# Optimization experiments

Hardware: AMD Instinct MI355X
Metric: run time of the kernel (lower is better)

Reference implementation:

```python
import jax, jax.numpy as jnp
import numpy as np

N, L, H, DH = 4, 1024, 16, 64
D = H * DH  # 1024
DFF = 4 * D
NEG_INF = jnp.float32(-1e30)  # used via actual -inf per torch masked_fill


def layer_norm(x, g, b, eps=1e-5):
    mu = jnp.mean(x, axis=-1, keepdims=True)
    var = jnp.mean(jnp.square(x - mu), axis=-1, keepdims=True)
    return (x - mu) * jax.lax.rsqrt(var + eps) * g + b


def mha(q_in, k_in, Wq, Wk, Wv, mask, padding_mask):
    # q_in: (N,Lq,D), k_in: (N,Lk,D); Linear weights (D,D), out = x @ W.T
    n, Lq, _ = q_in.shape
    Lk = k_in.shape[1]
    q = jnp.einsum('nld,od->nlo', q_in, Wq).reshape(n, Lq, H, DH)
    k = jnp.einsum('nld,od->nlo', k_in, Wk).reshape(n, Lk, H, DH)
    v = jnp.einsum('nld,od->nlo', k_in, Wv).reshape(n, Lk, H, DH)
    # per-sample scaling = sqrt(#non-padded keys)
    scaling = jnp.sqrt(jnp.sum(~padding_mask, axis=-1).astype(q.dtype))  # (N,)
    score = jnp.einsum('nqhd,nkhd->nhqk', q, k) / scaling[:, None, None, None]
    if mask is not None:
        score = jnp.where(mask[None, None, :, :], -jnp.inf, score)
    score = jnp.where(padding_mask[:, None, None, :], -jnp.inf, score)
    p = jax.nn.softmax(score, axis=-1)
    out = jnp.einsum('nhqk,nkhd->nqhd', p, v).reshape(n, Lq, D)
    return out


def setup_inputs() -> dict:
    key = jax.random.key(0)
    ks = jax.random.split(key, 16)
    s = 0.02
    inp = {
        'encoded': jax.random.normal(ks[0], (N, L, D), jnp.float32),
        'Y': jax.random.normal(ks[1], (N, L, D), jnp.float32),
        # causal mask: True above diagonal -> attention set to -inf
        'mask': ~jnp.tril(jnp.ones((L, L), dtype=bool)),
        # suffix padding with varied per-sample lengths (all >= 1)
        'padding_mask': jnp.arange(L)[None, :] >= jnp.array([L, 3 * L // 4, L // 2, 7 * L // 8])[:, None],
        # masked self-attention projections
        'Wq1': jax.random.normal(ks[2], (D, D), jnp.float32) * s,
        'Wk1': jax.random.normal(ks[3], (D, D), jnp.float32) * s,
        'Wv1': jax.random.normal(ks[4], (D, D), jnp.float32) * s,
        'g1': jnp.ones((D,), jnp.float32), 'b1': jnp.zeros((D,), jnp.float32),
        # cross-attention projections
        'Wq2': jax.random.normal(ks[5], (D, D), jnp.float32) * s,
        'Wk2': jax.random.normal(ks[6], (D, D), jnp.float32) * s,
        'Wv2': jax.random.normal(ks[7], (D, D), jnp.float32) * s,
        'g2': jnp.ones((D,), jnp.float32), 'b2': jnp.zeros((D,), jnp.float32),
        # FFN
        'We': jax.random.normal(ks[8], (DFF, D), jnp.float32) * s,
        'be': jnp.zeros((DFF,), jnp.float32),
        'Wc': jax.random.normal(ks[9], (D, DFF), jnp.float32) * s,
        'bc': jnp.zeros((D,), jnp.float32),
        'g3': jnp.ones((D,), jnp.float32), 'b3': jnp.zeros((D,), jnp.float32),
    }
    return inp


def reference(encoded, Y, mask, padding_mask,
              Wq1, Wk1, Wv1, g1, b1,
              Wq2, Wk2, Wv2, g2, b2,
              We, be, Wc, bc, g3, b3):
    # masked self-attention + residual + LN (dropout=0 -> identity)
    res = Y
    a = mha(Y, Y, Wq1, Wk1, Wv1, mask, padding_mask)
    Y = layer_norm(a + res, g1, b1)
    # cross-attention (no causal mask) + residual + LN
    res = Y
    a = mha(Y, encoded, Wq2, Wk2, Wv2, None, padding_mask)
    Y = layer_norm(a + res, g2, b2)
    # FFN + residual + LN
    res = Y
    h = jax.nn.relu(jnp.einsum('nld,fd->nlf', Y, We) + be)
    h = jnp.einsum('nlf,df->nld', h, Wc) + bc
    Y = layer_norm(h + res, g3, b3)
    return Y
```

## Files before the change

### kernel.cpp

```cpp
#include <hip/hip_runtime.h>
#include <stdint.h>

#define NB 4
#define LS 1024
#define HH 16
#define DHD 64
#define DM 1024
#define DF 4096
#define QKS 2048

typedef unsigned short u16;
typedef __attribute__((ext_vector_type(4))) float f32x4;
typedef __attribute__((ext_vector_type(8))) __bf16 bf16x8;
typedef __attribute__((ext_vector_type(8))) unsigned short u16x8;

__device__ __forceinline__ u16 f2bf(float f) {
  union { float f; uint32_t u; } v; v.f = f;
  uint32_t u = v.u;
  return (u16)((u + 0x7fffu + ((u >> 16) & 1u)) >> 16);
}

__device__ __forceinline__ bf16x8 ldb8(const u16* p) {
  u16x8 r = *(const u16x8*)p;
  return __builtin_bit_cast(bf16x8, r);
}

__device__ __forceinline__ void gload_lds16(const u16* g, u16* l) {
  __builtin_amdgcn_global_load_lds((const __attribute__((address_space(1))) void*)g,
                                   (__attribute__((address_space(3))) void*)l,
                                   16, 0, 0);
}

#define WAITV8() asm volatile("s_waitcnt vmcnt(8)" ::: "memory")
#define WAITV0() asm volatile("s_waitcnt vmcnt(0)" ::: "memory")
#define WAITLGKM() asm volatile("s_waitcnt lgkmcnt(0)" ::: "memory")
#define PHASE_BARRIER()                        \
  do {                                         \
    WAITLGKM();                                \
    __builtin_amdgcn_sched_barrier(0);         \
    __builtin_amdgcn_s_barrier();              \
    __builtin_amdgcn_sched_barrier(0);         \
  } while (0)

__global__ void prep_kernel(const uint32_t* __restrict__ pm, int* lens, float* iscl) {
  __shared__ int flagByte;
  __shared__ int red[256];
  const int tid = threadIdx.x, n = blockIdx.x;
  if (tid == 0) flagByte = 0;
  __syncthreads();
  int f = 0;
  for (int w = tid; w < (NB * LS) / 4; w += 256) {
    uint32_t u = pm[w];
    if (u != 0u && u != 1u && u != 0x3f800000u) f = 1;
  }
  if (f) atomicOr(&flagByte, 1);
  __syncthreads();
  int c = 0;
  if (flagByte) {
    const uint8_t* pb = (const uint8_t*)pm;
    for (int l = tid; l < LS; l += 256) c += (pb[n * LS + l] == 0) ? 1 : 0;
  } else {
    for (int l = tid; l < LS; l += 256) c += (pm[n * LS + l] == 0) ? 1 : 0;
  }
  red[tid] = c;
  __syncthreads();
  for (int s = 128; s > 0; s >>= 1) {
    if (tid < s) red[tid] += red[tid + s];
    __syncthreads();
  }
  if (tid == 0) { lens[n] = red[0]; iscl[n] = 1.0f / sqrtf((float)red[0]); }
}

__global__ void cvt_all(const float* s0, u16* d0, const float* s1, u16* d1,
                        const float* s2, u16* d2, const float* s3, u16* d3,
                        const float* s4, u16* d4, const float* s5, u16* d5,
                        const float* s6, u16* d6, const float* s7, u16* d7,
                        const float* s8, u16* d8, const float* s9, u16* d9) {
  const int total = 5767168;
  int i = blockIdx.x * 256 + threadIdx.x;
  for (; i < total; i += gridDim.x * 256) {
    const float* s; u16* d; int j;
    if (i < 1048576)      { s = s0; d = d0; j = i; }
    else if (i < 2097152) { s = s1; d = d1; j = i - 1048576; }
    else if (i < 2359296) { s = s2; d = d2; j = i - 2097152; }
    else if (i < 2621440) { s = s3; d = d3; j = i - 2359296; }
    else if (i < 2883584) { s = s4; d = d4; j = i - 2621440; }
    else if (i < 3145728) { s = s5; d = d5; j = i - 2883584; }
    else if (i < 3407872) { s = s6; d = d6; j = i - 3145728; }
    else if (i < 3670016) { s = s7; d = d7; j = i - 3407872; }
    else if (i < 4718592) { s = s8; d = d8; j = i - 3670016; }
    else                  { s = s9; d = d9; j = i - 4718592; }
    float4 fv = ((const float4*)s)[j];
    ushort4 o;
    o.x = f2bf(fv.x); o.y = f2bf(fv.y); o.z = f2bf(fv.z); o.w = f2bf(fv.w);
    ((ushort4*)d)[j] = o;
  }
}

template <int MODE>
__global__ __launch_bounds__(512, 2) void gemm8(
    const u16* __restrict__ P0, const u16* __restrict__ P1,
    const u16* __restrict__ PW, const float* __restrict__ bias,
    void* __restrict__ O0, void* __restrict__ O1,
    void* __restrict__ O2, void* __restrict__ O3) {
  extern __shared__ u16 lds[];
  constexpr int NT = 16;
  const int bm = blockIdx.x;
  const int tid = threadIdx.x;
  const int wid = tid >> 6, lane = tid & 63;
  const int lrow = lane & 15, lgrp = lane >> 4;
  const int wm = wid >> 2, wn = wid & 3;

  const u16* Asrc; const u16* Bsrc; int lda, ldb;
  if constexpr (MODE == 0) {
    Asrc = P0 + (size_t)bm * 256 * DM; lda = DM;
    Bsrc = PW + (size_t)blockIdx.y * 256 * DM; ldb = DM;
  } else if constexpr (MODE == 1) {
    const int z = blockIdx.z;
    Asrc = P0 + (size_t)bm * 256 * DF + z * 1024; lda = DF;
    Bsrc = PW + (size_t)blockIdx.y * 256 * DF + z * 1024; ldb = DF;
  } else {
    const int bnt = blockIdx.y;
    Asrc = (bnt < 12 ? P0 : P1) + (size_t)bm * 256 * DM; lda = DM;
    const int wrow = (bnt < 12) ? bnt * 256 : 4096 + (bnt - 12) * 256;
    Bsrc = PW + (size_t)wrow * DM; ldb = DM;
  }

  int srow[2], skk[2];
#pragma unroll
  for (int i = 0; i < 2; i++) {
    const int c = (i * 8 + wid) * 64 + lane;
    const int pair = c >> 3;
    const int ue = ((c & 7) * 8) ^ ((pair & 7) << 3);
    srow[i] = pair * 2 + (ue >> 5);
    skk[i] = ue & 31;
  }
  const int dslot0 = wid * 512;
  const int dslot1 = (8 + wid) * 512;

  f32x4 acc[2][4][4] = {};

  auto STAGE_A = [&](int kt, int buf, int kh) {
    const int ks = kt < NT ? kt : NT - 1;
    gload_lds16(Asrc + (size_t)srow[0] * lda + ks * 64 + kh * 32 + skk[0],
                lds + buf * 16384 + kh * 8192 + dslot0);
    gload_lds16(Asrc + (size_t)srow[1] * lda + ks * 64 + kh * 32 + skk[1],
                lds + buf * 16384 + kh * 8192 + dslot1);
  };
  auto STAGE_B = [&](int kt, int buf, int kh) {
    const int ks = kt < NT ? kt : NT - 1;
    gload_lds16(Bsrc + (size_t)srow[0] * ldb + ks * 64 + kh * 32 + skk[0],
                lds + 32768 + buf * 16384 + kh * 8192 + dslot0);
    gload_lds16(Bsrc + (size_t)srow[1] * ldb + ks * 64 + kh * 32 + skk[1],
                lds + 32768 + buf * 16384 + kh * 8192 + dslot1);
  };
  auto LDA = [&](int buf, int kh, int mh, bf16x8* a) {
#pragma unroll
    for (int m = 0; m < 4; m++) {
      const int row = wm * 128 + mh * 64 + m * 16 + lrow;
      const int idx = buf * 16384 + kh * 8192 + (row >> 1) * 64 +
                      ((((row & 1) << 5) + (lgrp << 3)) ^ (((row >> 1) & 7) << 3));
      a[m] = ldb8(lds + idx);
    }
  };
  auto LDB = [&](int buf, int kh, bf16x8* b) {
#pragma unroll
    for (int nn = 0; nn < 4; nn++) {
      const int row = wn * 64 + nn * 16 + lrow;
      const int idx = 32768 + buf * 16384 + kh * 8192 + (row >> 1) * 64 +
                      ((((row & 1) << 5) + (lgrp << 3)) ^ (((row >> 1) & 7) << 3));
      b[nn] = ldb8(lds + idx);
    }
  };
  auto MFMA16 = [&](f32x4 (&a4)[4][4], bf16x8* af, bf16x8* bk) {
    __builtin_amdgcn_s_setprio(1);
#pragma unroll
    for (int m = 0; m < 4; m++)
#pragma unroll
      for (int nn = 0; nn < 4; nn++)
        a4[m][nn] = __builtin_amdgcn_mfma_f32_16x16x32_bf16(af[m], bk[nn], a4[m][nn], 0, 0, 0);
    __builtin_amdgcn_s_setprio(0);
  };

  STAGE_A(0, 0, 0); STAGE_B(0, 0, 0);
  STAGE_A(0, 0, 1); STAGE_B(0, 0, 1);
  STAGE_A(1, 1, 0); STAGE_B(1, 1, 0);
  WAITV8();
  __builtin_amdgcn_s_barrier();
  __builtin_amdgcn_sched_barrier(0);

  for (int t = 0; t < NT; t++) {
    const int b = t & 1;
    bf16x8 af[4], bk[4];
    LDA(b, 0, 0, af); LDB(b, 0, bk);
    STAGE_A(t + 1, b ^ 1, 1);
    PHASE_BARRIER();
    MFMA16(acc[0], af, bk);
    LDA(b, 0, 1, af);
    STAGE_B(t + 1, b ^ 1, 1);
    WAITV8();
    PHASE_BARRIER();
    MFMA16(acc[1], af, bk);
    LDA(b, 1, 0, af); LDB(b, 1, bk);
    STAGE_A(t + 2, b, 0);
    PHASE_BARRIER();
    MFMA16(acc[0], af, bk);
    LDA(b, 1, 1, af);
    STAGE_B(t + 2, b, 0);
    WAITV8();
    PHASE_BARRIER();
    MFMA16(acc[1], af, bk);
  }
  WAITV0();

#pragma unroll
  for (int mh = 0; mh < 2; mh++)
#pragma unroll
    for (int m = 0; m < 4; m++) {
      const int grow0 = bm * 256 + wm * 128 + mh * 64 + m * 16 + lgrp * 4;
#pragma unroll
      for (int nn = 0; nn < 4; nn++) {
        const int col_l = wn * 64 + nn * 16 + lrow;
        f32x4 v = acc[mh][m][nn];
        if constexpr (MODE == 0) {
          const int col = blockIdx.y * 256 + col_l;
          const float bv = bias[col];
#pragma unroll
          for (int r = 0; r < 4; r++) {
            float x = v[r] + bv;
            x = x > 0.0f ? x : 0.0f;
            ((u16*)O0)[(size_t)(grow0 + r) * DF + col] = f2bf(x);
          }
        } else if constexpr (MODE == 1) {
          float* C = (float*)O0 + (size_t)blockIdx.z * ((size_t)NB * LS * DM);
          const int col = blockIdx.y * 256 + col_l;
#pragma unroll
          for (int r = 0; r < 4; r++) C[(size_t)(grow0 + r) * DM + col] = v[r];
        } else {
          const int bnt = blockIdx.y;
          const int nidx = grow0 >> 10, l0 = grow0 & 1023;
          if (bnt < 8) {
            const int col = bnt * 256 + col_l;
#pragma unroll
            for (int r = 0; r < 4; r++)
              ((u16*)O0)[(size_t)(grow0 + r) * QKS + col] = f2bf(v[r]);
          } else if (bnt < 12) {
            const int vc = (bnt - 8) * 256 + col_l;
            ushort4 o;
            o.x = f2bf(v[0]); o.y = f2bf(v[1]); o.z = f2bf(v[2]); o.w = f2bf(v[3]);
            *(ushort4*)((u16*)O1 + (((size_t)(nidx * HH + (vc >> 6)) * DHD + (vc & 63)) << 10) + l0) = o;
          } else {
            const int col = 1024 + (bnt - 12) * 256 + col_l;
#pragma unroll
            for (int r = 0; r < 4; r++)
              ((u16*)O2)[(size_t)(grow0 + r) * QKS + col] = f2bf(v[r]);
          }
        }
      }
    }
}

__global__ __launch_bounds__(256) void gemm_qv(const u16* __restrict__ Ya,
                                               const u16* __restrict__ Ea,
                                               const u16* __restrict__ Wq,
                                               const u16* __restrict__ Wv,
                                               u16* __restrict__ QKb,
                                               u16* __restrict__ VtB) {
  __shared__ u16 Al[128 * 32];
  __shared__ u16 Bl[128 * 32];
  const int tid = threadIdx.x;
  const int bm = blockIdx.x, bnr = blockIdx.y;
  const bool isV = bnr >= 8;
  const int bn = isV ? bnr - 8 : bnr;
  const int wave = tid >> 6, lane = tid & 63;
  const int lrow = lane & 15, lgrp = lane >> 4;
  const int wr = (wave >> 1) * 64, wc = (wave & 1) * 64;
  f32x4 acc[4][4] = {};
  const u16* Ab = (isV ? Ea : Ya) + (size_t)bm * 128 * DM;
  const u16* Bb = (isV ? Wv : Wq) + (size_t)bn * 128 * DM;
  {
    const int c0 = wave, c1 = wave + 4;
    const int r0 = c0 * 16 + (lane >> 2), r1 = c1 * 16 + (lane >> 2);
    const int scc = (lane & 3) * 8;
    const u16* Ag0 = Ab + (size_t)r0 * DM + scc;
    const u16* Ag1 = Ab + (size_t)r1 * DM + scc;
    const u16* Bg0 = Bb + (size_t)r0 * DM + scc;
    const u16* Bg1 = Bb + (size_t)r1 * DM + scc;
    u16* Ad0 = Al + c0 * 512;
    u16* Ad1 = Al + c1 * 512;
    u16* Bd0 = Bl + c0 * 512;
    u16* Bd1 = Bl + c1 * 512;
    for (int kb = 0; kb < DM; kb += 32) {
      gload_lds16(Ag0, Ad0);
      gload_lds16(Ag1, Ad1);
      gload_lds16(Bg0, Bd0);
      gload_lds16(Bg1, Bd1);
      Ag0 += 32; Ag1 += 32; Bg0 += 32; Bg1 += 32;
      __syncthreads();
      bf16x8 af[4], bfr[4];
#pragma unroll
      for (int m = 0; m < 4; m++) af[m] = ldb8(Al + (wr + m * 16 + lrow) * 32 + lgrp * 8);
#pragma unroll
      for (int nn = 0; nn < 4; nn++) bfr[nn] = ldb8(Bl + (wc + nn * 16 + lrow) * 32 + lgrp * 8);
#pragma unroll
      for (int m = 0; m < 4; m++)
#pragma unroll
        for (int nn = 0; nn < 4; nn++)
          acc[m][nn] = __builtin_amdgcn_mfma_f32_16x16x32_bf16(af[m], bfr[nn], acc[m][nn], 0, 0, 0);
      __syncthreads();
    }
  }
#pragma unroll
  for (int m = 0; m < 4; m++) {
    const int row0 = bm * 128 + wr + m * 16 + lgrp * 4;
    const int nidx = row0 >> 10, l0 = row0 & (LS - 1);
#pragma unroll
    for (int nn = 0; nn < 4; nn++) {
      const int col = bn * 128 + wc + nn * 16 + lrow;
      if (!isV) {
#pragma unroll
        for (int r = 0; r < 4; r++)
          QKb[(size_t)(row0 + r) * QKS + col] = f2bf(acc[m][nn][r]);
      } else {
        const int hh = col >> 6, dd = col & 63;
        ushort4 o;
        o.x = f2bf(acc[m][nn][0]); o.y = f2bf(acc[m][nn][1]);
        o.z = f2bf(acc[m][nn][2]); o.w = f2bf(acc[m][nn][3]);
        *(ushort4*)(VtB + (((size_t)(nidx * HH + hh) * DHD + dd) << 10) + l0) = o;
      }
    }
  }
}

template <bool CAUSAL>
__global__ __launch_bounds__(256) void attn_kernel(const u16* __restrict__ QK,
                                                   const u16* __restrict__ Vt,
                                                   float* __restrict__ Out,
                                                   const int* __restrict__ lens,
                                                   const float* __restrict__ iscl) {
  __shared__ u16 Kl[64 * 72];
  __shared__ u16 Vl[64 * 72];
  __shared__ u16 Pl[4][16 * 72];
  const int n = blockIdx.z, h = blockIdx.y, qb = blockIdx.x * 64;
  const int tid = threadIdx.x, wave = tid >> 6, lane = tid & 63;
  const int lrow = lane & 15, lgrp = lane >> 4;
  const int len = lens[n];
  const float isc = iscl[n];
  const int qrow = qb + wave * 16 + lrow;
  const u16* qptr = QK + ((size_t)(n * LS + qrow)) * QKS + h * DHD + lgrp * 8;
  bf16x8 qf0 = ldb8(qptr);
  bf16x8 qf1 = ldb8(qptr + 32);
  f32x4 oacc[4] = {};
  float m_run[4], l_run[4];
#pragma unroll
  for (int r = 0; r < 4; r++) { m_run[r] = -1e30f; l_run[r] = 0.0f; }
  const int kend = CAUSAL ? (len < qb + 64 ? len : qb + 64) : len;
  const int srow = tid >> 3, sc = (tid & 7) * 8;
  const u16* kg_base = QK + 1024 + ((size_t)(n * LS)) * QKS + h * DHD + sc;
  const u16* vg_base = Vt + ((size_t)((n * HH + h) * DHD) + srow) * LS + sc;
  u16* pw = Pl[wave];
  for (int kb = 0; kb < kend; kb += 64) {
    __syncthreads();
#pragma unroll
    for (int i = 0; i < 2; i++) {
      const int row = srow + i * 32;
      u16x8 kv = *(const u16x8*)(kg_base + (size_t)(kb + row) * QKS);
      *(u16x8*)(Kl + row * 72 + sc) = kv;
      u16x8 vv = *(const u16x8*)(vg_base + (size_t)(i * 32) * LS + kb);
      *(u16x8*)(Vl + row * 72 + sc) = vv;
    }
    __syncthreads();
    f32x4 s[4];
#pragma unroll
    for (int st = 0; st < 4; st++) {
      const u16* kr = Kl + (st * 16 + lrow) * 72 + lgrp * 8;
      bf16x8 kf0 = ldb8(kr);
      bf16x8 kf1 = ldb8(kr + 32);
      f32x4 z = {};
      z = __builtin_amdgcn_mfma_f32_16x16x32_bf16(qf0, kf0, z, 0, 0, 0);
      s[st] = __builtin_amdgcn_mfma_f32_16x16x32_bf16(qf1, kf1, z, 0, 0, 0);
    }
    const int q_r = qb + wave * 16 + lgrp * 4;
#pragma unroll
    for (int st = 0; st < 4; st++) {
      const int k = kb + st * 16 + lrow;
#pragma unroll
      for (int r = 0; r < 4; r++) {
        float v = s[st][r] * isc;
        bool ok = (k < len) && (!CAUSAL || k <= q_r + r);
        s[st][r] = ok ? v : -1e30f;
      }
    }
#pragma unroll
    for (int r = 0; r < 4; r++) {
      float mx = fmaxf(fmaxf(s[0][r], s[1][r]), fmaxf(s[2][r], s[3][r]));
      mx = fmaxf(mx, __shfl_xor(mx, 1));
      mx = fmaxf(mx, __shfl_xor(mx, 2));
      mx = fmaxf(mx, __shfl_xor(mx, 4));
      mx = fmaxf(mx, __shfl_xor(mx, 8));
      float mn = fmaxf(m_run[r], mx);
      float fac = __expf(m_run[r] - mn);
      m_run[r] = mn;
      float sm = 0.0f;
#pragma unroll
      for (int st = 0; st < 4; st++) {
        float p = __expf(s[st][r] - mn);
        s[st][r] = p;
        sm += p;
      }
      sm += __shfl_xor(sm, 1);
      sm += __shfl_xor(sm, 2);
      sm += __shfl_xor(sm, 4);
      sm += __shfl_xor(sm, 8);
      l_run[r] = l_run[r] * fac + sm;
#pragma unroll
      for (int dt = 0; dt < 4; dt++) oacc[dt][r] *= fac;
    }
#pragma unroll
    for (int st = 0; st < 4; st++)
#pragma unroll
      for (int r = 0; r < 4; r++)
        pw[(lgrp * 4 + r) * 72 + st * 16 + lrow] = f2bf(s[st][r]);
#pragma unroll
    for (int ks = 0; ks < 2; ks++) {
      bf16x8 pf = ldb8(pw + lrow * 72 + ks * 32 + lgrp * 8);
#pragma unroll
      for (int dt = 0; dt < 4; dt++) {
        bf16x8 vf = ldb8(Vl + (dt * 16 + lrow) * 72 + ks * 32 + lgrp * 8);
        oacc[dt] = __builtin_amdgcn_mfma_f32_16x16x32_bf16(pf, vf, oacc[dt], 0, 0, 0);
      }
    }
  }
#pragma unroll
  for (int r = 0; r < 4; r++) {
    float inv = 1.0f / l_run[r];
    const int row = qb + wave * 16 + lgrp * 4 + r;
    float* op = Out + ((size_t)(n * LS + row)) * DM + h * DHD;
#pragma unroll
    for (int dt = 0; dt < 4; dt++) op[dt * 16 + lrow] = oacc[dt][r] * inv;
  }
}

__global__ __launch_bounds__(256) void ln_kernel(const float* __restrict__ a,
                                                 const float* __restrict__ res,
                                                 const float* __restrict__ g,
                                                 const float* __restrict__ bta,
                                                 float* __restrict__ outf,
                                                 u16* __restrict__ outb) {
  const int row = blockIdx.x, tid = threadIdx.x;
  float4 x = ((const float4*)(a + (size_t)row * DM))[tid];
  float4 rr = ((const float4*)(res + (size_t)row * DM))[tid];
  x.x += rr.x; x.y += rr.y; x.z += rr.z; x.w += rr.w;
  float s = x.x + x.y + x.z + x.w;
  float s2 = x.x * x.x + x.y * x.y + x.z * x.z + x.w * x.w;
#pragma unroll
  for (int m = 1; m < 64; m <<= 1) { s += __shfl_xor(s, m); s2 += __shfl_xor(s2, m); }
  __shared__ float sm[8];
  const int wv = tid >> 6;
  if ((tid & 63) == 0) { sm[wv] = s; sm[4 + wv] = s2; }
  __syncthreads();
  s = sm[0] + sm[1] + sm[2] + sm[3];
  s2 = sm[4] + sm[5] + sm[6] + sm[7];
  const float mean = s * (1.0f / (float)DM);
  const float var = s2 * (1.0f / (float)DM) - mean * mean;
  const float inv = rsqrtf(var + 1e-5f);
  float4 gg = ((const float4*)g)[tid];
  float4 bb = ((const float4*)bta)[tid];
  float4 y;
  y.x = (x.x - mean) * inv * gg.x + bb.x;
  y.y = (x.y - mean) * inv * gg.y + bb.y;
  y.z = (x.z - mean) * inv * gg.z + bb.z;
  y.w = (x.w - mean) * inv * gg.w + bb.w;
  ((float4*)(outf + (size_t)row * DM))[tid] = y;
  if (outb) {
    ushort4 o;
    o.x = f2bf(y.x); o.y = f2bf(y.y); o.z = f2bf(y.z); o.w = f2bf(y.w);
    ((ushort4*)(outb + (size_t)row * DM))[tid] = o;
  }
}

__global__ __launch_bounds__(256) void ln_final(const float* __restrict__ part,
                                                const float* __restrict__ bias,
                                                const float* __restrict__ res,
                                                const float* __restrict__ g,
                                                const float* __restrict__ bta,
                                                float* __restrict__ outf) {
  const int row = blockIdx.x, tid = threadIdx.x;
  const size_t PS = (size_t)NB * LS * DM;
  float4 x = ((const float4*)(part + (size_t)row * DM))[tid];
  float4 p1 = ((const float4*)(part + PS + (size_t)row * DM))[tid];
  float4 p2 = ((const float4*)(part + 2 * PS + (size_t)row * DM))[tid];
  float4 p3 = ((const float4*)(part + 3 * PS + (size_t)row * DM))[tid];
  float4 bb4 = ((const float4*)bias)[tid];
  float4 rr = ((const float4*)(res + (size_t)row * DM))[tid];
  x.x += p1.x + p2.x + p3.x + bb4.x + rr.x;
  x.y += p1.y + p2.y + p3.y + bb4.y + rr.y;
  x.z += p1.z + p2.z + p3.z + bb4.z + rr.z;
  x.w += p1.w + p2.w + p3.w + bb4.w + rr.w;
  float s = x.x + x.y + x.z + x.w;
  float s2 = x.x * x.x + x.y * x.y + x.z * x.z + x.w * x.w;
#pragma unroll
  for (int m = 1; m < 64; m <<= 1) { s += __shfl_xor(s, m); s2 += __shfl_xor(s2, m); }
  __shared__ float sm[8];
  const int wv = tid >> 6;
  if ((tid & 63) == 0) { sm[wv] = s; sm[4 + wv] = s2; }
  __syncthreads();
  s = sm[0] + sm[1] + sm[2] + sm[3];
  s2 = sm[4] + sm[5] + sm[6] + sm[7];
  const float mean = s * (1.0f / (float)DM);
  const float var = s2 * (1.0f / (float)DM) - mean * mean;
  const float inv = rsqrtf(var + 1e-5f);
  float4 gg = ((const float4*)g)[tid];
  float4 bb = ((const float4*)bta)[tid];
  float4 y;
  y.x = (x.x - mean) * inv * gg.x + bb.x;
  y.y = (x.y - mean) * inv * gg.y + bb.y;
  y.z = (x.z - mean) * inv * gg.z + bb.z;
  y.w = (x.w - mean) * inv * gg.w + bb.w;
  ((float4*)(outf + (size_t)row * DM))[tid] = y;
}

extern "C" void kernel_launch(void* const* d_in, const int* in_sizes, int n_in,
                              void* d_out, int out_size, void* d_ws, size_t ws_size,
                              hipStream_t stream) {
  const float* enc = (const float*)d_in[0];
  const float* Yin = (const float*)d_in[1];
  const uint32_t* pmask = (const uint32_t*)d_in[3];
  const float* Wq1 = (const float*)d_in[4];
  const float* Wk1 = (const float*)d_in[5];
  const float* Wv1 = (const float*)d_in[6];
  const float* g1 = (const float*)d_in[7];
  const float* b1 = (const float*)d_in[8];
  const float* Wq2 = (const float*)d_in[9];
  const float* Wk2 = (const float*)d_in[10];
  const float* Wv2 = (const float*)d_in[11];
  const float* g2 = (const float*)d_in[12];
  const float* b2 = (const float*)d_in[13];
  const float* We = (const float*)d_in[14];
  const float* be = (const float*)d_in[15];
  const float* Wc = (const float*)d_in[16];
  const float* bc = (const float*)d_in[17];
  const float* g3 = (const float*)d_in[18];
  const float* b3 = (const float*)d_in[19];

  const size_t ACT = (size_t)NB * LS * DM;
  const size_t WSZ = (size_t)DM * DM;
  const size_t WFF = (size_t)DF * DM;
  const size_t HID = (size_t)NB * LS * DF;

  char* ws = (char*)d_ws;
  size_t off = 0;
  auto alloc = [&](size_t bytes) -> void* {
    void* p = ws + off;
    off += (bytes + 255) & ~(size_t)255;
    return p;
  };
  int* lens = (int*)alloc(64);
  float* iscl = (float*)alloc(64);
  u16* Ybf = (u16*)alloc(ACT * 2);
  u16* Ebf = (u16*)alloc(ACT * 2);
  u16* W6 = (u16*)alloc(WSZ * 6 * 2);
  u16* Web = (u16*)alloc(WFF * 2);
  u16* Wcb = (u16*)alloc(WFF * 2);
  size_t region0 = off;
  u16* QKa = (u16*)alloc((size_t)NB * LS * QKS * 2);
  u16* VtA = (u16*)alloc(ACT * 2);
  u16* QKb = (u16*)alloc((size_t)NB * LS * QKS * 2);
  u16* VtB = (u16*)alloc(ACT * 2);
  float* aout = (float*)alloc(ACT * 4);
  float* y2 = (float*)alloc(ACT * 4);
  float* part = (float*)(ws + region0);
  float* y3 = (float*)alloc(ACT * 4);
  u16* Hb = (u16*)alloc(HID * 2);

  prep_kernel<<<NB, 256, 0, stream>>>(pmask, lens, iscl);
  cvt_all<<<2048, 256, 0, stream>>>(Yin, Ybf, enc, Ebf,
                                    Wq1, W6 + 0 * WSZ, Wk1, W6 + 1 * WSZ,
                                    Wv1, W6 + 2 * WSZ, Wq2, W6 + 3 * WSZ,
                                    Wk2, W6 + 4 * WSZ, Wv2, W6 + 5 * WSZ,
                                    We, Web, Wc, Wcb);

  dim3 blk(256);
  gemm8<2><<<dim3(16, 16), 512, 131072, stream>>>(Ybf, Ebf, W6, nullptr,
                                                  QKa, VtA, QKb, VtB);
  attn_kernel<true><<<dim3(16, 16, 4), blk, 0, stream>>>(QKa, VtA, aout, lens, iscl);
  ln_kernel<<<NB * LS, 256, 0, stream>>>(aout, Yin, g1, b1, y2, Ybf);
  gemm_qv<<<dim3(32, 16), blk, 0, stream>>>(Ybf, Ebf, W6 + 3 * WSZ, W6 + 5 * WSZ,
                                            QKb, VtB);
  attn_kernel<false><<<dim3(16, 16, 4), blk, 0, stream>>>(QKb, VtB, aout, lens, iscl);
  ln_kernel<<<NB * LS, 256, 0, stream>>>(aout, y2, g2, b2, y3, Ebf);
  gemm8<0><<<dim3(16, 16), 512, 131072, stream>>>(Ebf, nullptr, Web, be,
                                                  Hb, nullptr, nullptr, nullptr);
  gemm8<1><<<dim3(16, 4, 4), 512, 131072, stream>>>(Hb, nullptr, Wcb, nullptr,
                                                    part, nullptr, nullptr, nullptr);
  ln_final<<<NB * LS, 256, 0, stream>>>(part, bc, y3, g3, b3, (float*)d_out);
}
```

Baseline: 319.0 us.

## Transpose QK^T MFMA layout and add lazy softmax rescaling in attention

Swaps the MFMA operand order so each lane holds one query row's scores across keys. Row max and sum then need only two cross-lane shuffles, and the running max and sum become scalars per lane. Adds a wave-uniform skip of the max update and accumulator rescale when the new max stays within a threshold of the running max, which trades exponent headroom for fewer rescales. P is packed to bf16 with hardware pack-convert instructions and written as vectorized LDS stores.

```diff
diff --git a/kernel.cpp b/kernel.cpp
--- a/kernel.cpp
+++ b/kernel.cpp
@@ -351,9 +351,7 @@
   bf16x8 qf0 = ldb8(qptr);
   bf16x8 qf1 = ldb8(qptr + 32);
   f32x4 oacc[4] = {};
-  float m_run[4], l_run[4];
-#pragma unroll
-  for (int r = 0; r < 4; r++) { m_run[r] = -1e30f; l_run[r] = 0.0f; }
+  float m_run = -1e30f, l_run = 0.0f;
   const int kend = CAUSAL ? (len < qb + 64 ? len : qb + 64) : len;
   const int srow = tid >> 3, sc = (tid & 7) * 8;
   const u16* kg_base = QK + 1024 + ((size_t)(n * LS)) * QKS + h * DHD + sc;
@@ -377,50 +375,61 @@
       bf16x8 kf0 = ldb8(kr);
       bf16x8 kf1 = ldb8(kr + 32);
       f32x4 z = {};
-      z = __builtin_amdgcn_mfma_f32_16x16x32_bf16(qf0, kf0, z, 0, 0, 0);
-      s[st] = __builtin_amdgcn_mfma_f32_16x16x32_bf16(qf1, kf1, z, 0, 0, 0);
-    }
-    const int q_r = qb + wave * 16 + lgrp * 4;
+      z = __builtin_amdgcn_mfma_f32_16x16x32_bf16(kf0, qf0, z, 0, 0, 0);
+      s[st] = __builtin_amdgcn_mfma_f32_16x16x32_bf16(kf1, qf1, z, 0, 0, 0);
+    }
 #pragma unroll
     for (int st = 0; st < 4; st++) {
-      const int k = kb + st * 16 + lrow;
 #pragma unroll
       for (int r = 0; r < 4; r++) {
+        const int k = kb + st * 16 + lgrp * 4 + r;
         float v = s[st][r] * isc;
-        bool ok = (k < len) && (!CAUSAL || k <= q_r + r);
+        bool ok = (k < len) && (!CAUSAL || k <= qrow);
         s[st][r] = ok ? v : -1e30f;
       }
     }
-#pragma unroll
-    for (int r = 0; r < 4; r++) {
-      float mx = fmaxf(fmaxf(s[0][r], s[1][r]), fmaxf(s[2][r], s[3][r]));
-      mx = fmaxf(mx, __shfl_xor(mx, 1));
-      mx = fmaxf(mx, __shfl_xor(mx, 2));
-      mx = fmaxf(mx, __shfl_xor(mx, 4));
-      mx = fmaxf(mx, __shfl_xor(mx, 8));
-      float mn = fmaxf(m_run[r], mx);
-      float fac = __expf(m_run[r] - mn);
-      m_run[r] = mn;
-      float sm = 0.0f;
-#pragma unroll
-      for (int st = 0; st < 4; st++) {
-        float p = __expf(s[st][r] - mn);
+    float pmax = s[0][0];
+#pragma unroll
+    for (int st = 0; st < 4; st++)
+#pragma unroll
+      for (int r = 0; r < 4; r++) pmax = fmaxf(pmax, s[st][r]);
+    pmax = fmaxf(pmax, __shfl_xor(pmax, 16));
+    pmax = fmaxf(pmax, __shfl_xor(pmax, 32));
+    const bool skip = __all(pmax <= m_run + 8.0f);
+    float fac = 1.0f;
+    if (!skip) {
+      float mn = fmaxf(m_run, pmax);
+      fac = __expf(m_run - mn);
+      m_run = mn;
+    }
+    float sm = 0.0f;
+#pragma unroll
+    for (int st = 0; st < 4; st++)
+#pragma unroll
+      for (int r = 0; r < 4; r++) {
+        float p = __expf(s[st][r] - m_run);
         s[st][r] = p;
         sm += p;
       }
-      sm += __shfl_xor(sm, 1);
-      sm += __shfl_xor(sm, 2);
-      sm += __shfl_xor(sm, 4);
-      sm += __shfl_xor(sm, 8);
-      l_run[r] = l_run[r] * fac + sm;
-#pragma unroll
-      for (int dt = 0; dt < 4; dt++) oacc[dt][r] *= fac;
-    }
-#pragma unroll
-    for (int st = 0; st < 4; st++)
-#pragma unroll
-      for (int r = 0; r < 4; r++)
-        pw[(lgrp * 4 + r) * 72 + st * 16 + lrow] = f2bf(s[st][r]);
+    sm += __shfl_xor(sm, 16);
+    sm += __shfl_xor(sm, 32);
+    l_run = l_run * fac + sm;
+    if (!skip) {
+#pragma unroll
+      for (int r = 0; r < 4; r++) {
+        float fr = __shfl(fac, (lane & 48) | (lgrp * 4 + r));
+#pragma unroll
+        for (int dt = 0; dt < 4; dt++) oacc[dt][r] *= fr;
+      }
+    }
+#pragma unroll
+    for (int st = 0; st < 4; st++) {
+      uint32_t w0, w1;
+      asm("v_cvt_pk_bf16_f32 %0, %1, %2" : "=v"(w0) : "v"(s[st][0]), "v"(s[st][1]));
+      asm("v_cvt_pk_bf16_f32 %0, %1, %2" : "=v"(w1) : "v"(s[st][2]), "v"(s[st][3]));
+      uint2 wv; wv.x = w0; wv.y = w1;
+      *(uint2*)(pw + lrow * 72 + st * 16 + lgrp * 4) = wv;
+    }
 #pragma unroll
     for (int ks = 0; ks < 2; ks++) {
       bf16x8 pf = ldb8(pw + lrow * 72 + ks * 32 + lgrp * 8);
@@ -433,7 +442,8 @@
   }
 #pragma unroll
   for (int r = 0; r < 4; r++) {
-    float inv = 1.0f / l_run[r];
+    float lr = __shfl(l_run, (lane & 48) | (lgrp * 4 + r));
+    float inv = 1.0f / lr;
     const int row = qb + wave * 16 + lgrp * 4 + r;
     float* op = Out + ((size_t)(n * LS + row)) * DM + h * DHD;
 #pragma unroll
```

Result: faster. 297.8 us (-6.7%).
